# Kernel tuning notes

Measured on AMD Instinct MI355X. Metric: run time of the kernel, lower is better.

The kernel has to match this reference:

```python
import jax, jax.numpy as jnp
import numpy as np


def _mlp(x, W1, b1, W2, b2, W3, b3, W4, b4, W5, b5):
    # x: [..., 3] -> [..., 12]
    h = jax.nn.silu(x @ W1 + b1)
    h = jax.nn.silu(h @ W2 + b2)
    h = jax.nn.silu(h @ W3 + b3)
    h = jax.nn.silu(h @ W4 + b4)
    return h @ W5 + b5


def setup_inputs() -> dict:
    key = jax.random.key(0)
    ks = jax.random.split(key, 11)
    N = 1_000_000
    s = lambda k, shp, fan: jax.random.normal(k, shp, dtype=jnp.float32) * (1.0 / np.sqrt(fan))
    return {
        "x": jax.random.normal(ks[0], (N, 3), dtype=jnp.float32),
        "W1": s(ks[1], (3, 64), 3), "b1": jnp.zeros((64,), jnp.float32),
        "W2": s(ks[2], (64, 64), 64), "b2": jnp.zeros((64,), jnp.float32),
        "W3": s(ks[3], (64, 64), 64), "b3": jnp.zeros((64,), jnp.float32),
        "W4": s(ks[4], (64, 64), 64), "b4": jnp.zeros((64,), jnp.float32),
        "W5": s(ks[5], (64, 12), 64), "b5": jnp.zeros((12,), jnp.float32),
    }


def reference(x, W1, b1, W2, b2, W3, b3, W4, b4, W5, b5):
    # Full Jacobian d field / d x per point, via 3 fused forward-mode (JVP) passes
    # (input dim 3 < output dim 12, so forward mode is optimal).
    N = x.shape[0]
    f = lambda xx: _mlp(xx, W1, b1, W2, b2, W3, b3, W4, b4, W5, b5)
    eye = jnp.eye(3, dtype=x.dtype)

    def jvp_dir(t):  # t: [3] basis direction
        return jax.jvp(f, (x,), (jnp.broadcast_to(t, x.shape),))[1]  # [N, 12]

    jac = jax.vmap(jvp_dir)(eye)             # [3(partial), N, 12]
    jac = jnp.transpose(jac, (1, 0, 2))      # [N, partialxyz=3, 12]
    # 12 -> (xyz=3, reim=2, eb=2), matching einops rearrange 'n p (xyz reim eb)'
    return jac.reshape(N, 3, 3, 2, 2)
```

## Files before the change

kernel.cpp:

```cpp
#include <hip/hip_runtime.h>
#include <hip/hip_bf16.h>


#define THREADS 256

typedef float  f32x16 __attribute__((ext_vector_type(16)));
typedef float  f32x4  __attribute__((ext_vector_type(4)));
typedef short  s16x8  __attribute__((ext_vector_type(8)));

#define MFMA(a, b, c) __builtin_amdgcn_mfma_f32_32x32x16_bf16(a, b, c, 0, 0, 0)

__device__ __forceinline__ uint cvtpk(float a, float b) {
    uint r;
    asm("v_cvt_pk_bf16_f32 %0, %1, %2" : "=v"(r) : "v"(a), "v"(b));
    return r;
}
__device__ __forceinline__ void plswap(uint &a, uint &b) {
    asm("v_permlane32_swap_b32 %0, %1" : "+v"(a), "+v"(b));
}
__device__ __forceinline__ float quad0(float v) {
    return __int_as_float(__builtin_amdgcn_mov_dpp(__float_as_int(v), 0, 0xF, 0xF, false));
}
__device__ __forceinline__ ushort bfhi(float v) {
    uint u = __float_as_uint(v);
    return (ushort)((u + 0x7FFFu + ((u >> 16) & 1u)) >> 16);
}
__device__ __forceinline__ s16x8 mk8(uint a, uint b, uint c, uint d) {
    union { uint u[4]; s16x8 s; } x;
    x.u[0] = a; x.u[1] = b; x.u[2] = c; x.u[3] = d;
    return x.s;
}
__device__ __forceinline__ void pack_pairs(const f32x16 &A, const int i0,
                                           uint (&H)[4], uint (&L)[4]) {
    #pragma unroll
    for (int q = 0; q < 4; ++q) {
        float v0 = A[i0 + 2 * q], v1 = A[i0 + 2 * q + 1];
        uint  Hc = cvtpk(v0, v1);
        float r0 = v0 - __uint_as_float(Hc << 16);
        float r1 = v1 - __uint_as_float(Hc & 0xFFFF0000u);
        H[q] = Hc;
        L[q] = cvtpk(r0, r1);
    }
    plswap(H[0], H[2]); plswap(H[1], H[3]);
    plswap(L[0], L[2]); plswap(L[1], L[3]);
}

__global__ __launch_bounds__(THREADS, 4)
void PartialDerivatives_mfma(const float* __restrict__ x,
                             const float* __restrict__ W1, const float* __restrict__ b1,
                             const float* __restrict__ W2, const float* __restrict__ b2,
                             const float* __restrict__ W3, const float* __restrict__ b3,
                             const float* __restrict__ W4, const float* __restrict__ b4,
                             const float* __restrict__ W5,
                             float* __restrict__ out, int N, int ntiles)
{
    __shared__ __align__(16) ushort sWH[3 * 2 * 4 * 64 * 8];
    __shared__ __align__(16) ushort sW1[2 * 64 * 8];
    __shared__ __align__(16) ushort sW5[4 * 64 * 8];
    __shared__ __align__(16) float  sB[4 * 64];
    __shared__ __align__(8)  float2 sTab[2][513];

    const int tid = threadIdx.x;
    for (int i = tid; i < 12288; i += THREADS) {
        int e = i & 7, lane = (i >> 3) & 63, kk = (i >> 9) & 3, mt = (i >> 11) & 1, l = i >> 12;
        int n = mt * 32 + (lane & 31);
        int k = kk * 16 + (lane >> 5) * 8 + e;
        const float* W = (l == 0) ? W2 : (l == 1) ? W3 : W4;
        sWH[i] = bfhi(W[k * 64 + n]);
    }
    for (int i = tid; i < 1024; i += THREADS) {
        int e = i & 7, lane = (i >> 3) & 63, mt = i >> 9;
        int n = mt * 32 + (lane & 31);
        int k = (lane >> 5) * 8 + e;
        sW1[i] = (k < 3) ? bfhi(W1[k * 64 + n]) : (ushort)0;
    }
    for (int i = tid; i < 2048; i += THREADS) {
        int e = i & 7, lane = (i >> 3) & 63, kk = i >> 9;
        int m = lane & 31;
        int k = kk * 16 + (lane >> 5) * 8 + e;
        sW5[i] = (m < 12) ? bfhi(W5[k * 12 + m]) : (ushort)0;
    }
    if (tid < 64) {
        sB[tid] = b1[tid]; sB[64 + tid] = b2[tid];
        sB[128 + tid] = b3[tid]; sB[192 + tid] = b4[tid];
    }
    for (int i = tid; i < 1026; i += THREADS) {
        int  c  = (i >= 513);
        int  k  = c ? i - 513 : i;
        float z0 = -10.f + k * 0.0390625f;
        float z1 = z0 + 0.0390625f;
        float s0 = 1.f / (1.f + __expf(-z0));
        float s1 = 1.f / (1.f + __expf(-z1));
        float y0 = c ? s0 * (1.f + z0 * (1.f - s0)) : s0;
        float y1 = c ? s1 * (1.f + z1 * (1.f - s1)) : s1;
        sTab[c][k] = make_float2(y0, y1 - y0);
    }
    __syncthreads();

    const int  lane = tid & 63;
    const int  hi   = lane >> 5;
    const int  s    = lane & 3;
    const bool is0  = (s == 0);
    const int  pq   = (lane & 31) >> 2;
    const float2* __restrict__ tb = &sTab[is0 ? 0 : 1][0];

    const int wid = blockIdx.x * (THREADS / 64) + (tid >> 6);
    const int nw  = gridDim.x * (THREADS / 64);

#define SILU16(A)                                                              \
    { _Pragma("unroll")                                                        \
      for (int i = 0; i < 16; ++i) {                                           \
          float zb = quad0(A[i]);                                              \
          float zc = fminf(fmaxf(zb, -10.f), 10.f);                            \
          float u  = __builtin_fmaf(zc, 25.6f, 256.0f);                        \
          float fl = floorf(u);                                                \
          float fr = u - fl;                                                   \
          float2 e = tb[(int)fl];                                              \
          A[i] *= __builtin_fmaf(e.y, fr, e.x);                                \
      } }

#define EPILOGUE_NT(nt, aLo, aHi)                                              \
    {   SILU16(aLo); SILU16(aHi);                                              \
        pack_pairs(aLo, 0, Bh[0][nt], Bl[0][nt]);                              \
        pack_pairs(aLo, 8, Bh[1][nt], Bl[1][nt]);                              \
        pack_pairs(aHi, 0, Bh[2][nt], Bl[2][nt]);                              \
        pack_pairs(aHi, 8, Bh[3][nt], Bl[3][nt]); }

#define BINIT(boff, aLo, aHi)                                                  \
    { _Pragma("unroll")                                                        \
      for (int q = 0; q < 4; ++q) {                                            \
          f32x4 bb0 = *(const f32x4*)&sB[(boff) + q * 8 + hi * 4];             \
          f32x4 bb1 = *(const f32x4*)&sB[(boff) + 32 + q * 8 + hi * 4];        \
          _Pragma("unroll")                                                    \
          for (int j = 0; j < 4; ++j) {                                        \
              aLo[q * 4 + j] = bb0[j]; aHi[q * 4 + j] = bb1[j];                \
          } } }

    #pragma unroll 1
    for (int t = wid; t < ntiles; t += nw) {
        const int base = t * 16;
        uint Bh[4][2][4], Bl[4][2][4];

        #pragma unroll
        for (int nt = 0; nt < 2; ++nt) {
            f32x16 aLo, aHi;
            BINIT(0, aLo, aHi);
            uint h0 = 0u, h1 = 0u, l0 = 0u, l1 = 0u;
            if (hi == 0) {
                if (is0) {
                    int pt = base + nt * 8 + pq;
                    if (pt > N - 1) pt = N - 1;
                    const float* xp = x + (size_t)pt * 3;
                    float x0 = xp[0], x1 = xp[1], x2 = xp[2];
                    h0 = cvtpk(x0, x1);
                    h1 = cvtpk(x2, 0.f);
                    float r0 = x0 - __uint_as_float(h0 << 16);
                    float r1 = x1 - __uint_as_float(h0 & 0xFFFF0000u);
                    float r2 = x2 - __uint_as_float(h1 << 16);
                    l0 = cvtpk(r0, r1); l1 = cvtpk(r2, 0.f);
                } else {
                    h0 = (s == 1) ? 0x3F80u : (s == 2) ? 0x3F800000u : 0u;
                    h1 = (s == 3) ? 0x3F80u : 0u;
                }
            }
            s16x8 A0  = *(const s16x8*)&sW1[0 * 512 + lane * 8];
            s16x8 A1  = *(const s16x8*)&sW1[1 * 512 + lane * 8];
            s16x8 bh  = mk8(h0, h1, 0u, 0u);
            s16x8 bl  = mk8(l0, l1, 0u, 0u);
            aLo = MFMA(A0, bh, aLo); aLo = MFMA(A0, bl, aLo);
            aHi = MFMA(A1, bh, aHi); aHi = MFMA(A1, bl, aHi);
            EPILOGUE_NT(nt, aLo, aHi);
        }

        #pragma unroll 1
        for (int l = 0; l < 3; ++l) {
            #pragma unroll
            for (int nt = 0; nt < 2; ++nt) {
                f32x16 aLo, aHi;
                BINIT((l + 1) * 64, aLo, aHi);
                #pragma unroll
                for (int kk = 0; kk < 4; ++kk) {
                    s16x8 A0 = *(const s16x8*)&sWH[((l * 2 + 0) * 4 + kk) * 512 + lane * 8];
                    s16x8 A1 = *(const s16x8*)&sWH[((l * 2 + 1) * 4 + kk) * 512 + lane * 8];
                    s16x8 bh = mk8(Bh[kk][nt][0], Bh[kk][nt][1], Bh[kk][nt][2], Bh[kk][nt][3]);
                    s16x8 bl = mk8(Bl[kk][nt][0], Bl[kk][nt][1], Bl[kk][nt][2], Bl[kk][nt][3]);
                    aLo = MFMA(A0, bh, aLo); aLo = MFMA(A0, bl, aLo);
                    aHi = MFMA(A1, bh, aHi); aHi = MFMA(A1, bl, aHi);
                }
                EPILOGUE_NT(nt, aLo, aHi);
            }
        }

        #pragma unroll
        for (int nt = 0; nt < 2; ++nt) {
            f32x16 o;
            #pragma unroll
            for (int i = 0; i < 16; ++i) o[i] = 0.f;
            #pragma unroll
            for (int kk = 0; kk < 4; ++kk) {
                s16x8 A5 = *(const s16x8*)&sW5[kk * 512 + lane * 8];
                s16x8 bh = mk8(Bh[kk][nt][0], Bh[kk][nt][1], Bh[kk][nt][2], Bh[kk][nt][3]);
                s16x8 bl = mk8(Bl[kk][nt][0], Bl[kk][nt][1], Bl[kk][nt][2], Bl[kk][nt][3]);
                o = MFMA(A5, bh, o); o = MFMA(A5, bl, o);
            }
            if (!is0) {
                int pt = base + nt * 8 + pq;
                if (pt < N) {
                    float* ob = out + (size_t)pt * 36 + (s - 1) * 12;
                    if (hi == 0) {
                        *(f32x4*)(ob + 0) = (f32x4){o[0], o[1], o[2], o[3]};
                        *(f32x4*)(ob + 8) = (f32x4){o[4], o[5], o[6], o[7]};
                    } else {
                        *(f32x4*)(ob + 4) = (f32x4){o[0], o[1], o[2], o[3]};
                    }
                }
            }
        }
    }
#undef SILU16
#undef EPILOGUE_NT
#undef BINIT
}

extern "C" void kernel_launch(void* const* d_in, const int* in_sizes, int n_in,
                              void* d_out, int out_size, void* d_ws, size_t ws_size,
                              hipStream_t stream) {
    const float* x  = (const float*)d_in[0];
    const float* W1 = (const float*)d_in[1];
    const float* b1 = (const float*)d_in[2];
    const float* W2 = (const float*)d_in[3];
    const float* b2 = (const float*)d_in[4];
    const float* W3 = (const float*)d_in[5];
    const float* b3 = (const float*)d_in[6];
    const float* W4 = (const float*)d_in[7];
    const float* b4 = (const float*)d_in[8];
    const float* W5 = (const float*)d_in[9];
    float* out = (float*)d_out;

    const int N = in_sizes[0] / 3;
    const int ntiles = (N + 15) / 16;
    const int blocks = 2048;
    PartialDerivatives_mfma<<<blocks, THREADS, 0, stream>>>(
        x, W1, b1, W2, b2, W3, b3, W4, b4, W5, out, N, ntiles);
}
```

Before: 684.8 us.

## Process each 8-point subtile through all layers before the next

Reorders the loop nest so each of the two 8-point subtiles runs through every MLP layer and the output layer before the other starts, instead of interleaving subtiles within each layer. The bf16 hi/lo activation arrays shrink from two subtiles to one, which cuts VGPR pressure and may allow higher occupancy. In exchange, the two independent MFMA chains per layer are no longer interleaved, which reduces instruction-level parallelism, and the layer-weight LDS reads are repeated per subtile.

```diff
diff --git a/kernel.cpp b/kernel.cpp
--- a/kernel.cpp
+++ b/kernel.cpp
@@ -119,14 +119,14 @@
           A[i] *= __builtin_fmaf(e.y, fr, e.x);                                \
       } }
 
-#define EPILOGUE_NT(nt, aLo, aHi)                                              \
+#define EPILOGUE()                                                             \
     {   SILU16(aLo); SILU16(aHi);                                              \
-        pack_pairs(aLo, 0, Bh[0][nt], Bl[0][nt]);                              \
-        pack_pairs(aLo, 8, Bh[1][nt], Bl[1][nt]);                              \
-        pack_pairs(aHi, 0, Bh[2][nt], Bl[2][nt]);                              \
-        pack_pairs(aHi, 8, Bh[3][nt], Bl[3][nt]); }
-
-#define BINIT(boff, aLo, aHi)                                                  \
+        pack_pairs(aLo, 0, Bh[0], Bl[0]);                                      \
+        pack_pairs(aLo, 8, Bh[1], Bl[1]);                                      \
+        pack_pairs(aHi, 0, Bh[2], Bl[2]);                                      \
+        pack_pairs(aHi, 8, Bh[3], Bl[3]); }
+
+#define BINIT(boff)                                                            \
     { _Pragma("unroll")                                                        \
       for (int q = 0; q < 4; ++q) {                                            \
           f32x4 bb0 = *(const f32x4*)&sB[(boff) + q * 8 + hi * 4];             \
@@ -139,68 +139,64 @@
     #pragma unroll 1
     for (int t = wid; t < ntiles; t += nw) {
         const int base = t * 16;
-        uint Bh[4][2][4], Bl[4][2][4];
 
         #pragma unroll
         for (int nt = 0; nt < 2; ++nt) {
+            uint Bh[4][4], Bl[4][4];
             f32x16 aLo, aHi;
-            BINIT(0, aLo, aHi);
-            uint h0 = 0u, h1 = 0u, l0 = 0u, l1 = 0u;
-            if (hi == 0) {
-                if (is0) {
-                    int pt = base + nt * 8 + pq;
-                    if (pt > N - 1) pt = N - 1;
-                    const float* xp = x + (size_t)pt * 3;
-                    float x0 = xp[0], x1 = xp[1], x2 = xp[2];
-                    h0 = cvtpk(x0, x1);
-                    h1 = cvtpk(x2, 0.f);
-                    float r0 = x0 - __uint_as_float(h0 << 16);
-                    float r1 = x1 - __uint_as_float(h0 & 0xFFFF0000u);
-                    float r2 = x2 - __uint_as_float(h1 << 16);
-                    l0 = cvtpk(r0, r1); l1 = cvtpk(r2, 0.f);
-                } else {
-                    h0 = (s == 1) ? 0x3F80u : (s == 2) ? 0x3F800000u : 0u;
-                    h1 = (s == 3) ? 0x3F80u : 0u;
+
+            BINIT(0);
+            {
+                uint h0 = 0u, h1 = 0u, l0 = 0u, l1 = 0u;
+                if (hi == 0) {
+                    if (is0) {
+                        int pt = base + nt * 8 + pq;
+                        if (pt > N - 1) pt = N - 1;
+                        const float* xp = x + (size_t)pt * 3;
+                        float x0 = xp[0], x1 = xp[1], x2 = xp[2];
+                        h0 = cvtpk(x0, x1);
+                        h1 = cvtpk(x2, 0.f);
+                        float r0 = x0 - __uint_as_float(h0 << 16);
+                        float r1 = x1 - __uint_as_float(h0 & 0xFFFF0000u);
+                        float r2 = x2 - __uint_as_float(h1 << 16);
+                        l0 = cvtpk(r0, r1); l1 = cvtpk(r2, 0.f);
+                    } else {
+                        h0 = (s == 1) ? 0x3F80u : (s == 2) ? 0x3F800000u : 0u;
+                        h1 = (s == 3) ? 0x3F80u : 0u;
+                    }
                 }
-            }
-            s16x8 A0  = *(const s16x8*)&sW1[0 * 512 + lane * 8];
-            s16x8 A1  = *(const s16x8*)&sW1[1 * 512 + lane * 8];
-            s16x8 bh  = mk8(h0, h1, 0u, 0u);
-            s16x8 bl  = mk8(l0, l1, 0u, 0u);
-            aLo = MFMA(A0, bh, aLo); aLo = MFMA(A0, bl, aLo);
-            aHi = MFMA(A1, bh, aHi); aHi = MFMA(A1, bl, aHi);
-            EPILOGUE_NT(nt, aLo, aHi);
-        }
-
-        #pragma unroll 1
-        for (int l = 0; l < 3; ++l) {
-            #pragma unroll
-            for (int nt = 0; nt < 2; ++nt) {
-                f32x16 aLo, aHi;
-                BINIT((l + 1) * 64, aLo, aHi);
+                s16x8 A0 = *(const s16x8*)&sW1[0 * 512 + lane * 8];
+                s16x8 A1 = *(const s16x8*)&sW1[1 * 512 + lane * 8];
+                s16x8 bh = mk8(h0, h1, 0u, 0u);
+                s16x8 bl = mk8(l0, l1, 0u, 0u);
+                aLo = MFMA(A0, bh, aLo); aLo = MFMA(A0, bl, aLo);
+                aHi = MFMA(A1, bh, aHi); aHi = MFMA(A1, bl, aHi);
+            }
+            EPILOGUE();
+
+            #pragma unroll 1
+            for (int l = 0; l < 3; ++l) {
+                BINIT((l + 1) * 64);
                 #pragma unroll
                 for (int kk = 0; kk < 4; ++kk) {
                     s16x8 A0 = *(const s16x8*)&sWH[((l * 2 + 0) * 4 + kk) * 512 + lane * 8];
                     s16x8 A1 = *(const s16x8*)&sWH[((l * 2 + 1) * 4 + kk) * 512 + lane * 8];
-                    s16x8 bh = mk8(Bh[kk][nt][0], Bh[kk][nt][1], Bh[kk][nt][2], Bh[kk][nt][3]);
-                    s16x8 bl = mk8(Bl[kk][nt][0], Bl[kk][nt][1], Bl[kk][nt][2], Bl[kk][nt][3]);
+                    s16x8 bh = mk8(Bh[kk][0], Bh[kk][1], Bh[kk][2], Bh[kk][3]);
+                    s16x8 bl = mk8(Bl[kk][0], Bl[kk][1], Bl[kk][2], Bl[kk][3]);
                     aLo = MFMA(A0, bh, aLo); aLo = MFMA(A0, bl, aLo);
                     aHi = MFMA(A1, bh, aHi); aHi = MFMA(A1, bl, aHi);
                 }
-                EPILOGUE_NT(nt, aLo, aHi);
-            }
-        }
-
-        #pragma unroll
-        for (int nt = 0; nt < 2; ++nt) {
+                EPILOGUE();
+            }
+
             f32x16 o;
             #pragma unroll
             for (int i = 0; i < 16; ++i) o[i] = 0.f;
             #pragma unroll
             for (int kk = 0; kk < 4; ++kk) {
                 s16x8 A5 = *(const s16x8*)&sW5[kk * 512 + lane * 8];
-                s16x8 bh = mk8(Bh[kk][nt][0], Bh[kk][nt][1], Bh[kk][nt][2], Bh[kk][nt][3]);
-                s16x8 bl = mk8(Bl[kk][nt][0], Bl[kk][nt][1], Bl[kk][nt][2], Bl[kk][nt][3]);
+                s16x8 bh = mk8(Bh[kk][0], Bh[kk][1], Bh[kk][2], Bh[kk][3]);
+                s16x8 bl = mk8(Bl[kk][0], Bl[kk][1], Bl[kk][2], Bl[kk][3]);
                 o = MFMA(A5, bh, o); o = MFMA(A5, bl, o);
             }
             if (!is0) {
@@ -218,7 +214,7 @@
         }
     }
 #undef SILU16
-#undef EPILOGUE_NT
+#undef EPILOGUE
 #undef BINIT
 }
 
```

Result: faster. 618.4 us (-9.7%).
